# Kernel tuning notes

Measured on AMD Instinct MI355X. Metric: run time of the kernel, lower is better.

The kernel has to match this reference:

```python
import jax, jax.numpy as jnp
import numpy as np

HIDDEN_DIM = 1024
SEQ_LEN = 4096
D_IN = 1024


def setup_inputs() -> dict:
    key = jax.random.key(0)
    ks = jax.random.split(key, 9)
    s = 1.0 / np.sqrt(D_IN)
    return {
        "q": jax.random.normal(ks[0], (SEQ_LEN, D_IN), jnp.float32),
        "k": jax.random.normal(ks[1], (SEQ_LEN, D_IN), jnp.float32),
        "v": jax.random.normal(ks[2], (SEQ_LEN, D_IN), jnp.float32),
        "Wq": jax.random.normal(ks[3], (D_IN, HIDDEN_DIM), jnp.float32) * s,
        "bq": jnp.zeros((HIDDEN_DIM,), jnp.float32),
        "Wk": jax.random.normal(ks[4], (D_IN, HIDDEN_DIM), jnp.float32) * s,
        "bk": jnp.zeros((HIDDEN_DIM,), jnp.float32),
        "Wv": jax.random.normal(ks[5], (D_IN, HIDDEN_DIM), jnp.float32) * s,
        "bv": jnpp_zeros() if False else jnp.zeros((HIDDEN_DIM,), jnp.float32),
    }


def reference(q, k, v, Wq, bq, Wk, bk, Wv, bv):
    # Dense projections (flax Dense: x @ W + b)
    query = q @ Wq + bq          # [S, H]
    key_p = k @ Wk + bk          # [S, H]
    value = v @ Wv + bv          # [S, H]
    # scores = Q K^T / sqrt(hidden_dim)  -> [S, S]
    scores = jnp.matmul(query, key_p.T) / jnp.sqrt(jnp.float32(HIDDEN_DIM))
    weights = jax.nn.softmax(scores, axis=-1)
    context = jnp.matmul(weights, value)  # [S, H]
    return context
```

## Files before the change

### kernel.cpp

```cpp
#include <hip/hip_runtime.h>


typedef short short4v __attribute__((ext_vector_type(4)));
typedef short short8  __attribute__((ext_vector_type(8)));
typedef float f32x4   __attribute__((ext_vector_type(4)));

#define MFMA16 __builtin_amdgcn_mfma_f32_16x16x32_bf16

__device__ __forceinline__ short f2bf(float f) {
    union { float f; unsigned u; } x; x.f = f;
    unsigned r = (x.u + 0x7FFFu + ((x.u >> 16) & 1u)) >> 16;
    return (short)r;
}
__device__ __forceinline__ float bf2f(short s) {
    union { unsigned u; float f; } x;
    x.u = ((unsigned)(unsigned short)s) << 16; return x.f;
}
__device__ __forceinline__ void store_out(short* p, float v) { *p = f2bf(v); }
__device__ __forceinline__ void store_out(float* p, float v) { *p = v; }

__device__ __forceinline__ void gl2lds(const short* g, short* l) {
    __builtin_amdgcn_global_load_lds(
        (const __attribute__((address_space(1))) void*)g,
        (__attribute__((address_space(3))) void*)l, 16, 0, 0);
}

__global__ __launch_bounds__(256) void prep_w(
    const float* __restrict__ W0, const float* __restrict__ W1,
    const float* __restrict__ W2, short* __restrict__ Wt)
{
    __shared__ float tile[64][65];
    const float* W = blockIdx.z == 0 ? W0 : (blockIdx.z == 1 ? W1 : W2);
    short* T = Wt + (size_t)blockIdx.z * 1048576;
    const int c0 = blockIdx.x * 64;
    const int r0 = blockIdx.y * 64;
    const int tx = threadIdx.x & 63;
    const int ty = threadIdx.x >> 6;
    #pragma unroll
    for (int p = 0; p < 16; ++p) {
        int r = ty + p * 4;
        tile[r][tx] = W[(size_t)(r0 + r) * 1024 + c0 + tx];
    }
    __syncthreads();
    #pragma unroll
    for (int p = 0; p < 16; ++p) {
        int r = ty + p * 4;
        T[(size_t)(c0 + r) * 1024 + r0 + tx] = f2bf(tile[tx][r]);
    }
}

__global__ __launch_bounds__(256) void cast_qkv(
    const float* __restrict__ q, const float* __restrict__ k,
    const float* __restrict__ v, short* __restrict__ xb)
{
    const float* src = blockIdx.z == 0 ? q : (blockIdx.z == 1 ? k : v);
    short* dst = xb + (size_t)blockIdx.z * 4194304;
    for (int i = blockIdx.x * 256 + threadIdx.x; i < 1048576; i += 256 * 1024) {
        float4 f = ((const float4*)src)[i];
        short4v o;
        o[0] = f2bf(f.x); o[1] = f2bf(f.y); o[2] = f2bf(f.z); o[3] = f2bf(f.w);
        ((short4v*)dst)[i] = o;
    }
}

__global__ __launch_bounds__(256) void transpose_v(
    const short* __restrict__ src, short* __restrict__ dst)
{
    __shared__ short t[64][65];
    const int c0 = blockIdx.x * 64;
    const int r0 = blockIdx.y * 64;
    const int tx = threadIdx.x & 63;
    const int ty = threadIdx.x >> 6;
    #pragma unroll
    for (int p = 0; p < 16; ++p) {
        const int r = p * 4 + ty;
        t[r][tx] = src[(size_t)(r0 + r) * 1024 + c0 + tx];
    }
    __syncthreads();
    #pragma unroll
    for (int p = 0; p < 16; ++p) {
        const int r = p * 4 + ty;
        dst[(size_t)(c0 + r) * 4096 + r0 + tx] = t[tx][r];
    }
}

template <typename TOut, int MODE>
__global__ __launch_bounds__(512, 2) void gemm256(
    const short* __restrict__ A, const short* __restrict__ Bt,
    const float* __restrict__ b0, const float* __restrict__ b1,
    const float* __restrict__ b2,
    TOut* __restrict__ C, float* __restrict__ P1, float* __restrict__ P2,
    float* __restrict__ P3,
    int M, int N, int lda, int ldb, float scale,
    int nc, int nc_last, int kstep)
{
    __shared__ short Lds[65536];

    const int t    = threadIdx.x;
    const int lane = t & 63;
    const int wv   = t >> 6;

    int m0, n0;
    {
        const int nb  = gridDim.x;
        const int bid = blockIdx.y * nb + blockIdx.x;
        if (nb == 16 && gridDim.y == 16) {
            const int x = bid & 7, i = bid >> 3;
            m0 = ((x & 1) * 8 + (i & 7)) * 256;
            n0 = ((x >> 1) * 4 + (i >> 3)) * 256;
        } else {
            const int band   = bid / (8 * nb);
            const int within = bid - band * 8 * nb;
            m0 = (band * 8 + (within & 7)) * 256;
            n0 = (within >> 3) * 256;
        }
    }

    const float* bias = nullptr;
    int kbeg = 0;
    TOut* Cw = C;
    if constexpr (MODE == 1) {
        const int z = blockIdx.z;
        A  += (size_t)z * M * lda;
        Bt += (size_t)z * N * ldb;
        Cw  = C + (size_t)z * M * N;
        bias = z == 0 ? b0 : (z == 1 ? b1 : b2);
    }
    if constexpr (MODE == 2) {
        const int z = blockIdx.z;
        kbeg = z * kstep;
        if (z == (int)gridDim.z - 1) nc = nc_last;
        Cw = (TOut*)(z == 0 ? (float*)C : (z == 1 ? P1 : (z == 2 ? P2 : P3)));
    }
    (void)b0; (void)b1; (void)b2; (void)P1; (void)P2; (void)P3;
    (void)nc_last; (void)kstep;

    const int srow = lane >> 2;
    const int skof = (lane & 3) * 8;
    const short* pA0 = A  + (size_t)(m0 + wv * 16 + srow) * lda + kbeg + skof;
    const short* pA1 = pA0 + (size_t)128 * lda;
    const short* pB0 = Bt + (size_t)(n0 + wv * 16 + srow) * ldb + kbeg + skof;
    const short* pB1 = pB0 + (size_t)128 * ldb;
    short* sA0 = Lds + wv * 512;
    short* sA1 = Lds + 4096  + wv * 512;
    short* sB0 = Lds + 8192  + wv * 512;
    short* sB1 = Lds + 12288 + wv * 512;

    const int wm = wv >> 2, wn = wv & 3;
    const int lr = lane & 15, lq = lane >> 4;
    const short* rdA = Lds + (wm * 128 + lr) * 32 + lq * 8;
    const short* rdB = Lds + 8192 + (wn * 64 + lr) * 32 + lq * 8;

    f32x4 acc[8][4];
    #pragma unroll
    for (int i = 0; i < 8; ++i)
        #pragma unroll
        for (int j = 0; j < 4; ++j) { f32x4 z4 = {0.f,0.f,0.f,0.f}; acc[i][j] = z4; }

#define STAGE(c) {                                                        \
    const int su_ = (c) & 3;                                              \
    const size_t ko_ = (size_t)(c) * 32;                                  \
    gl2lds(pA0 + ko_, sA0 + su_ * 16384);                                 \
    gl2lds(pA1 + ko_, sA1 + su_ * 16384);                                 \
    gl2lds(pB0 + ko_, sB0 + su_ * 16384);                                 \
    gl2lds(pB1 + ko_, sB1 + su_ * 16384); }

    STAGE(0); STAGE(1); STAGE(2);
    asm volatile("s_waitcnt vmcnt(8)" ::: "memory");
    __builtin_amdgcn_s_barrier();

#define PHASE(c, DOSTAGE, VMN) {                                          \
    const int u_ = (c) & 3;                                               \
    const short* rA_ = rdA + u_ * 16384;                                  \
    const short* rB_ = rdB + u_ * 16384;                                  \
    short8 af[8], bfr[4];                                                 \
    _Pragma("unroll") for (int i = 0; i < 8; ++i)                         \
        af[i] = *(const short8*)(rA_ + i * 512);                          \
    _Pragma("unroll") for (int j = 0; j < 4; ++j)                         \
        bfr[j] = *(const short8*)(rB_ + j * 512);                         \
    if (DOSTAGE) STAGE((c) + 3);                                          \
    __builtin_amdgcn_s_barrier();                                         \
    __builtin_amdgcn_s_setprio(1);                                        \
    _Pragma("unroll") for (int i = 0; i < 8; ++i)                         \
        _Pragma("unroll") for (int j = 0; j < 4; ++j)                     \
            acc[i][j] = MFMA16(af[i], bfr[j], acc[i][j], 0, 0, 0);        \
    __builtin_amdgcn_s_setprio(0);                                        \
    if ((VMN) == 8)      asm volatile("s_waitcnt vmcnt(8)" ::: "memory"); \
    else if ((VMN) == 4) asm volatile("s_waitcnt vmcnt(4)" ::: "memory"); \
    else if ((VMN) == 0) asm volatile("s_waitcnt vmcnt(0)" ::: "memory"); \
    if ((VMN) >= 0) __builtin_amdgcn_s_barrier(); }

    #pragma unroll 4
    for (int c = 0; c < nc - 3; ++c) PHASE(c, 1, 8);
    PHASE(nc - 3, 0, 4);
    PHASE(nc - 2, 0, 0);
    PHASE(nc - 1, 0, -1);
#undef PHASE
#undef STAGE

    #pragma unroll
    for (int i = 0; i < 8; ++i) {
        const int crow = m0 + wm * 128 + i * 16 + lq * 4;
        #pragma unroll
        for (int j = 0; j < 4; ++j) {
            const int ccol = n0 + wn * 64 + j * 16 + lr;
            float bb = 0.f;
            if constexpr (MODE == 1) bb = bias[ccol];
            #pragma unroll
            for (int r = 0; r < 4; ++r) {
                float val = acc[i][j][r] * scale + bb;
                store_out(&Cw[(size_t)(crow + r) * N + ccol], val);
            }
        }
    }
}

__global__ __launch_bounds__(256) void softmax_bf16(short* __restrict__ S)
{
    const int row = blockIdx.x;
    short8* r8 = (short8*)(S + (size_t)row * 4096);
    const int t = threadIdx.x;

    float x[16];
    #pragma unroll
    for (int i = 0; i < 2; ++i) {
        short8 raw = r8[t + 256 * i];
        #pragma unroll
        for (int j = 0; j < 8; ++j) x[8 * i + j] = bf2f(raw[j]);
    }
    float m = -1e30f;
    #pragma unroll
    for (int i = 0; i < 16; ++i) m = fmaxf(m, x[i]);
    #pragma unroll
    for (int off = 32; off > 0; off >>= 1) m = fmaxf(m, __shfl_xor(m, off));

    __shared__ float redm[4], reds[4];
    const int wv = t >> 6;
    if ((t & 63) == 0) redm[wv] = m;
    __syncthreads();
    m = fmaxf(fmaxf(redm[0], redm[1]), fmaxf(redm[2], redm[3]));

    float s = 0.f;
    #pragma unroll
    for (int i = 0; i < 16; ++i) { x[i] = __expf(x[i] - m); s += x[i]; }
    #pragma unroll
    for (int off = 32; off > 0; off >>= 1) s += __shfl_xor(s, off);
    if ((t & 63) == 0) reds[wv] = s;
    __syncthreads();
    s = reds[0] + reds[1] + reds[2] + reds[3];
    const float inv = 1.f / s;

    #pragma unroll
    for (int i = 0; i < 2; ++i) {
        short8 o;
        #pragma unroll
        for (int j = 0; j < 8; ++j) o[j] = f2bf(x[8 * i + j] * inv);
        r8[t + 256 * i] = o;
    }
}

__global__ __launch_bounds__(256) void combine(
    float* __restrict__ out, const float* __restrict__ a,
    const float* __restrict__ b, const float* __restrict__ c, int np)
{
    for (int i = blockIdx.x * 256 + threadIdx.x; i < 1048576; i += 256 * 1024) {
        float4 o = ((const float4*)out)[i];
        float4 x = ((const float4*)a)[i];
        float4 y = ((const float4*)b)[i];
        o.x += x.x + y.x; o.y += x.y + y.y;
        o.z += x.z + y.z; o.w += x.w + y.w;
        if (np == 3) {
            float4 w = ((const float4*)c)[i];
            o.x += w.x; o.y += w.y; o.z += w.z; o.w += w.w;
        }
        ((float4*)out)[i] = o;
    }
}

extern "C" void kernel_launch(void* const* d_in, const int* in_sizes, int n_in,
                              void* d_out, int out_size, void* d_ws, size_t ws_size,
                              hipStream_t stream)
{
    const float* q  = (const float*)d_in[0];
    const float* k  = (const float*)d_in[1];
    const float* v  = (const float*)d_in[2];
    const float* Wq = (const float*)d_in[3];
    const float* bq = (const float*)d_in[4];
    const float* Wk = (const float*)d_in[5];
    const float* bk = (const float*)d_in[6];
    const float* Wv = (const float*)d_in[7];
    const float* bv = (const float*)d_in[8];
    float* out = (float*)d_out;

    char* ws = (char*)d_ws;
    const size_t MB = 1ull << 20;
    short* Wt = (short*)(ws + 0);
    short* xb = (short*)(ws + 6 * MB);
    short* pr = (short*)(ws + 30 * MB);
    short* S  = (short*)(ws + 46 * MB);
    short* Vt = (short*)(ws + 78 * MB);
    float* p1 = (float*)(ws + 0);
    float* p2 = (float*)(ws + 16 * MB);
    float* p3 = (float*)(ws + 86 * MB);
    const int SK = (ws_size >= 102 * MB) ? 4 : 3;

    prep_w<<<dim3(16, 16, 3), 256, 0, stream>>>(Wq, Wk, Wv, Wt);
    cast_qkv<<<dim3(1024, 1, 3), 256, 0, stream>>>(q, k, v, xb);
    gemm256<short, 1><<<dim3(4, 16, 3), 512, 0, stream>>>(
        xb, Wt, bq, bk, bv, pr, nullptr, nullptr, nullptr,
        4096, 1024, 1024, 1024, 1.f, 32, 32, 0);
    transpose_v<<<dim3(16, 64), 256, 0, stream>>>(pr + 8 * 1024 * 1024, Vt);
    gemm256<short, 0><<<dim3(16, 16), 512, 0, stream>>>(
        pr, pr + 4 * 1024 * 1024, nullptr, nullptr, nullptr, S,
        nullptr, nullptr, nullptr,
        4096, 4096, 1024, 1024, 0.03125f, 32, 32, 0);
    softmax_bf16<<<4096, 256, 0, stream>>>(S);
    if (SK == 4) {
        gemm256<float, 2><<<dim3(4, 16, 4), 512, 0, stream>>>(
            S, Vt, nullptr, nullptr, nullptr, out, p1, p2, p3,
            4096, 1024, 4096, 4096, 1.f, 32, 32, 1024);
        combine<<<1024, 256, 0, stream>>>(out, p1, p2, p3, 3);
    } else {
        gemm256<float, 2><<<dim3(4, 16, 3), 512, 0, stream>>>(
            S, Vt, nullptr, nullptr, nullptr, out, p1, p2, nullptr,
            4096, 1024, 4096, 4096, 1.f, 42, 44, 1344);
        combine<<<1024, 256, 0, stream>>>(out, p1, p2, nullptr, 2);
    }
}
```

Baseline: 259.6 us.

## Swizzle LDS tile layout and split GEMM phase into two half-A MFMA sub-phases

Applies an XOR swizzle to the 16-byte chunk column used by both the global-to-LDS loads and the LDS fragment reads, so fragment reads from LDS avoid bank conflicts. Each pipeline phase is also split into two halves. The first half loads four A fragments and issues the A prefetch, and the second half reloads the other four A fragments and issues the B prefetch. This cuts live fragment registers and interleaves global loads with MFMA work, at the cost of extra barriers per phase.

```diff
diff --git a/kernel.cpp b/kernel.cpp
--- a/kernel.cpp
+++ b/kernel.cpp
@@ -136,7 +136,7 @@
     (void)nc_last; (void)kstep;
 
     const int srow = lane >> 2;
-    const int skof = (lane & 3) * 8;
+    const int skof = ((lane & 3) ^ ((lane >> 3) & 3)) * 8;
     const short* pA0 = A  + (size_t)(m0 + wv * 16 + srow) * lda + kbeg + skof;
     const short* pA1 = pA0 + (size_t)128 * lda;
     const short* pB0 = Bt + (size_t)(n0 + wv * 16 + srow) * ldb + kbeg + skof;
@@ -148,8 +148,9 @@
 
     const int wm = wv >> 2, wn = wv & 3;
     const int lr = lane & 15, lq = lane >> 4;
-    const short* rdA = Lds + (wm * 128 + lr) * 32 + lq * 8;
-    const short* rdB = Lds + 8192 + (wn * 64 + lr) * 32 + lq * 8;
+    const int pcol = lq ^ ((lr >> 1) & 3);
+    const short* rdA = Lds + (wm * 128 + lr) * 32 + pcol * 8;
+    const short* rdB = Lds + 8192 + (wn * 64 + lr) * 32 + pcol * 8;
 
     f32x4 acc[8][4];
     #pragma unroll
@@ -157,15 +158,20 @@
         #pragma unroll
         for (int j = 0; j < 4; ++j) { f32x4 z4 = {0.f,0.f,0.f,0.f}; acc[i][j] = z4; }
 
-#define STAGE(c) {                                                        \
+#define STAGE_A(c) {                                                      \
     const int su_ = (c) & 3;                                              \
     const size_t ko_ = (size_t)(c) * 32;                                  \
     gl2lds(pA0 + ko_, sA0 + su_ * 16384);                                 \
-    gl2lds(pA1 + ko_, sA1 + su_ * 16384);                                 \
+    gl2lds(pA1 + ko_, sA1 + su_ * 16384); }
+#define STAGE_B(c) {                                                      \
+    const int su_ = (c) & 3;                                              \
+    const size_t ko_ = (size_t)(c) * 32;                                  \
     gl2lds(pB0 + ko_, sB0 + su_ * 16384);                                 \
     gl2lds(pB1 + ko_, sB1 + su_ * 16384); }
 
-    STAGE(0); STAGE(1); STAGE(2);
+    STAGE_A(0); STAGE_B(0);
+    STAGE_A(1); STAGE_B(1);
+    STAGE_A(2); STAGE_B(2);
     asm volatile("s_waitcnt vmcnt(8)" ::: "memory");
     __builtin_amdgcn_s_barrier();
 
@@ -173,17 +179,27 @@
     const int u_ = (c) & 3;                                               \
     const short* rA_ = rdA + u_ * 16384;                                  \
     const short* rB_ = rdB + u_ * 16384;                                  \
-    short8 af[8], bfr[4];                                                 \
-    _Pragma("unroll") for (int i = 0; i < 8; ++i)                         \
+    short8 af[4], bfr[4];                                                 \
+    _Pragma("unroll") for (int i = 0; i < 4; ++i)                         \
         af[i] = *(const short8*)(rA_ + i * 512);                          \
     _Pragma("unroll") for (int j = 0; j < 4; ++j)                         \
         bfr[j] = *(const short8*)(rB_ + j * 512);                         \
-    if (DOSTAGE) STAGE((c) + 3);                                          \
+    if (DOSTAGE) STAGE_A((c) + 3);                                        \
     __builtin_amdgcn_s_barrier();                                         \
     __builtin_amdgcn_s_setprio(1);                                        \
-    _Pragma("unroll") for (int i = 0; i < 8; ++i)                         \
+    _Pragma("unroll") for (int i = 0; i < 4; ++i)                         \
         _Pragma("unroll") for (int j = 0; j < 4; ++j)                     \
             acc[i][j] = MFMA16(af[i], bfr[j], acc[i][j], 0, 0, 0);        \
+    __builtin_amdgcn_s_setprio(0);                                        \
+    __builtin_amdgcn_s_barrier();                                         \
+    _Pragma("unroll") for (int i = 0; i < 4; ++i)                         \
+        af[i] = *(const short8*)(rA_ + (4 + i) * 512);                    \
+    if (DOSTAGE) STAGE_B((c) + 3);                                        \
+    __builtin_amdgcn_s_barrier();                                         \
+    __builtin_amdgcn_s_setprio(1);                                        \
+    _Pragma("unroll") for (int i = 0; i < 4; ++i)                         \
+        _Pragma("unroll") for (int j = 0; j < 4; ++j)                     \
+            acc[4 + i][j] = MFMA16(af[i], bfr[j], acc[4 + i][j], 0, 0, 0);\
     __builtin_amdgcn_s_setprio(0);                                        \
     if ((VMN) == 8)      asm volatile("s_waitcnt vmcnt(8)" ::: "memory"); \
     else if ((VMN) == 4) asm volatile("s_waitcnt vmcnt(4)" ::: "memory"); \
@@ -196,7 +212,8 @@
     PHASE(nc - 2, 0, 0);
     PHASE(nc - 1, 0, -1);
 #undef PHASE
-#undef STAGE
+#undef STAGE_A
+#undef STAGE_B
 
     #pragma unroll
     for (int i = 0; i < 8; ++i) {
```

Measured after the change: 253.3 us. -2.4%, faster.

## Shrink GEMM tile to 128x256 with double buffering and swizzled LDS

Applied to the files above, without the earlier changes.

Replaces the 256x256 GEMM tile with a 128x256 tile and cuts the accumulator array in half. The four-stage LDS ring becomes a two-stage double buffer using much less shared memory, and launch bounds rise to allow four blocks per CU. LDS column offsets are XOR-swizzled on both the write and read side to reduce bank conflicts. Grids double in the M dimension to give more blocks and better occupancy, at the cost of less data reuse per block, a shallower prefetch pipeline, and dropping the special 16x16 block-order remap used for the scores GEMM.

```diff
diff --git a/kernel.cpp b/kernel.cpp
--- a/kernel.cpp
+++ b/kernel.cpp
@@ -85,7 +85,7 @@
 }
 
 template <typename TOut, int MODE>
-__global__ __launch_bounds__(512, 2) void gemm256(
+__global__ __launch_bounds__(512, 4) void gemm128(
     const short* __restrict__ A, const short* __restrict__ Bt,
     const float* __restrict__ b0, const float* __restrict__ b1,
     const float* __restrict__ b2,
@@ -94,27 +94,18 @@
     int M, int N, int lda, int ldb, float scale,
     int nc, int nc_last, int kstep)
 {
-    __shared__ short Lds[65536];
+    __shared__ short Lds[24576];
 
     const int t    = threadIdx.x;
     const int lane = t & 63;
     const int wv   = t >> 6;
 
-    int m0, n0;
-    {
-        const int nb  = gridDim.x;
-        const int bid = blockIdx.y * nb + blockIdx.x;
-        if (nb == 16 && gridDim.y == 16) {
-            const int x = bid & 7, i = bid >> 3;
-            m0 = ((x & 1) * 8 + (i & 7)) * 256;
-            n0 = ((x >> 1) * 4 + (i >> 3)) * 256;
-        } else {
-            const int band   = bid / (8 * nb);
-            const int within = bid - band * 8 * nb;
-            m0 = (band * 8 + (within & 7)) * 256;
-            n0 = (within >> 3) * 256;
-        }
-    }
+    const int nb  = gridDim.x;
+    const int bid = blockIdx.y * nb + blockIdx.x;
+    const int band   = bid / (8 * nb);
+    const int within = bid - band * 8 * nb;
+    const int m0 = (band * 8 + (within & 7)) * 128;
+    const int n0 = (within >> 3) * 256;
 
     const float* bias = nullptr;
     int kbeg = 0;
@@ -136,71 +127,65 @@
     (void)nc_last; (void)kstep;
 
     const int srow = lane >> 2;
-    const int skof = (lane & 3) * 8;
-    const short* pA0 = A  + (size_t)(m0 + wv * 16 + srow) * lda + kbeg + skof;
-    const short* pA1 = pA0 + (size_t)128 * lda;
+    const int skof = ((lane & 3) ^ ((lane >> 3) & 3)) * 8;
+    const short* pA  = A  + (size_t)(m0 + wv * 16 + srow) * lda + kbeg + skof;
     const short* pB0 = Bt + (size_t)(n0 + wv * 16 + srow) * ldb + kbeg + skof;
     const short* pB1 = pB0 + (size_t)128 * ldb;
-    short* sA0 = Lds + wv * 512;
-    short* sA1 = Lds + 4096  + wv * 512;
-    short* sB0 = Lds + 8192  + wv * 512;
-    short* sB1 = Lds + 12288 + wv * 512;
+    short* sA  = Lds + wv * 512;
+    short* sB0 = Lds + 4096 + wv * 512;
+    short* sB1 = Lds + 8192 + wv * 512;
 
     const int wm = wv >> 2, wn = wv & 3;
     const int lr = lane & 15, lq = lane >> 4;
-    const short* rdA = Lds + (wm * 128 + lr) * 32 + lq * 8;
-    const short* rdB = Lds + 8192 + (wn * 64 + lr) * 32 + lq * 8;
-
-    f32x4 acc[8][4];
-    #pragma unroll
-    for (int i = 0; i < 8; ++i)
+    const int pcol = lq ^ ((lr >> 1) & 3);
+    const short* rdA = Lds + (wm * 64 + lr) * 32 + pcol * 8;
+    const short* rdB = Lds + 4096 + (wn * 64 + lr) * 32 + pcol * 8;
+
+    f32x4 acc[4][4];
+    #pragma unroll
+    for (int i = 0; i < 4; ++i)
         #pragma unroll
         for (int j = 0; j < 4; ++j) { f32x4 z4 = {0.f,0.f,0.f,0.f}; acc[i][j] = z4; }
 
 #define STAGE(c) {                                                        \
-    const int su_ = (c) & 3;                                              \
+    const int s_ = (c) & 1;                                               \
     const size_t ko_ = (size_t)(c) * 32;                                  \
-    gl2lds(pA0 + ko_, sA0 + su_ * 16384);                                 \
-    gl2lds(pA1 + ko_, sA1 + su_ * 16384);                                 \
-    gl2lds(pB0 + ko_, sB0 + su_ * 16384);                                 \
-    gl2lds(pB1 + ko_, sB1 + su_ * 16384); }
-
-    STAGE(0); STAGE(1); STAGE(2);
-    asm volatile("s_waitcnt vmcnt(8)" ::: "memory");
-    __builtin_amdgcn_s_barrier();
-
-#define PHASE(c, DOSTAGE, VMN) {                                          \
-    const int u_ = (c) & 3;                                               \
-    const short* rA_ = rdA + u_ * 16384;                                  \
-    const short* rB_ = rdB + u_ * 16384;                                  \
-    short8 af[8], bfr[4];                                                 \
-    _Pragma("unroll") for (int i = 0; i < 8; ++i)                         \
+    gl2lds(pA  + ko_, sA  + s_ * 12288);                                  \
+    gl2lds(pB0 + ko_, sB0 + s_ * 12288);                                  \
+    gl2lds(pB1 + ko_, sB1 + s_ * 12288); }
+
+#define COMPUTE(c) {                                                      \
+    const short* rA_ = rdA + ((c) & 1) * 12288;                           \
+    const short* rB_ = rdB + ((c) & 1) * 12288;                           \
+    short8 af[4], bf_[4];                                                 \
+    _Pragma("unroll") for (int i = 0; i < 4; ++i)                         \
         af[i] = *(const short8*)(rA_ + i * 512);                          \
     _Pragma("unroll") for (int j = 0; j < 4; ++j)                         \
-        bfr[j] = *(const short8*)(rB_ + j * 512);                         \
-    if (DOSTAGE) STAGE((c) + 3);                                          \
-    __builtin_amdgcn_s_barrier();                                         \
+        bf_[j] = *(const short8*)(rB_ + j * 512);                         \
     __builtin_amdgcn_s_setprio(1);                                        \
-    _Pragma("unroll") for (int i = 0; i < 8; ++i)                         \
+    _Pragma("unroll") for (int i = 0; i < 4; ++i)                         \
         _Pragma("unroll") for (int j = 0; j < 4; ++j)                     \
-            acc[i][j] = MFMA16(af[i], bfr[j], acc[i][j], 0, 0, 0);        \
-    __builtin_amdgcn_s_setprio(0);                                        \
-    if ((VMN) == 8)      asm volatile("s_waitcnt vmcnt(8)" ::: "memory"); \
-    else if ((VMN) == 4) asm volatile("s_waitcnt vmcnt(4)" ::: "memory"); \
-    else if ((VMN) == 0) asm volatile("s_waitcnt vmcnt(0)" ::: "memory"); \
-    if ((VMN) >= 0) __builtin_amdgcn_s_barrier(); }
-
-    #pragma unroll 4
-    for (int c = 0; c < nc - 3; ++c) PHASE(c, 1, 8);
-    PHASE(nc - 3, 0, 4);
-    PHASE(nc - 2, 0, 0);
-    PHASE(nc - 1, 0, -1);
-#undef PHASE
+            acc[i][j] = MFMA16(af[i], bf_[j], acc[i][j], 0, 0, 0);        \
+    __builtin_amdgcn_s_setprio(0); }
+
+    STAGE(0);
+
+    for (int c = 0; c < nc - 1; ++c) {
+        STAGE(c + 1);
+        asm volatile("s_waitcnt vmcnt(3)" ::: "memory");
+        __builtin_amdgcn_s_barrier();
+        COMPUTE(c);
+        __builtin_amdgcn_s_barrier();
+    }
+    asm volatile("s_waitcnt vmcnt(0)" ::: "memory");
+    __builtin_amdgcn_s_barrier();
+    COMPUTE(nc - 1);
+#undef COMPUTE
 #undef STAGE
 
     #pragma unroll
-    for (int i = 0; i < 8; ++i) {
-        const int crow = m0 + wm * 128 + i * 16 + lq * 4;
+    for (int i = 0; i < 4; ++i) {
+        const int crow = m0 + wm * 64 + i * 16 + lq * 4;
         #pragma unroll
         for (int j = 0; j < 4; ++j) {
             const int ccol = n0 + wn * 64 + j * 16 + lr;
@@ -306,22 +291,22 @@
 
     prep_w<<<dim3(16, 16, 3), 256, 0, stream>>>(Wq, Wk, Wv, Wt);
     cast_qkv<<<dim3(1024, 1, 3), 256, 0, stream>>>(q, k, v, xb);
-    gemm256<short, 1><<<dim3(4, 16, 3), 512, 0, stream>>>(
+    gemm128<short, 1><<<dim3(4, 32, 3), 512, 0, stream>>>(
         xb, Wt, bq, bk, bv, pr, nullptr, nullptr, nullptr,
         4096, 1024, 1024, 1024, 1.f, 32, 32, 0);
     transpose_v<<<dim3(16, 64), 256, 0, stream>>>(pr + 8 * 1024 * 1024, Vt);
-    gemm256<short, 0><<<dim3(16, 16), 512, 0, stream>>>(
+    gemm128<short, 0><<<dim3(16, 32), 512, 0, stream>>>(
         pr, pr + 4 * 1024 * 1024, nullptr, nullptr, nullptr, S,
         nullptr, nullptr, nullptr,
         4096, 4096, 1024, 1024, 0.03125f, 32, 32, 0);
     softmax_bf16<<<4096, 256, 0, stream>>>(S);
     if (SK == 4) {
-        gemm256<float, 2><<<dim3(4, 16, 4), 512, 0, stream>>>(
+        gemm128<float, 2><<<dim3(4, 32, 4), 512, 0, stream>>>(
             S, Vt, nullptr, nullptr, nullptr, out, p1, p2, p3,
             4096, 1024, 4096, 4096, 1.f, 32, 32, 1024);
         combine<<<1024, 256, 0, stream>>>(out, p1, p2, p3, 3);
     } else {
-        gemm256<float, 2><<<dim3(4, 16, 3), 512, 0, stream>>>(
+        gemm128<float, 2><<<dim3(4, 32, 3), 512, 0, stream>>>(
             S, Vt, nullptr, nullptr, nullptr, out, p1, p2, nullptr,
             4096, 1024, 4096, 4096, 1.f, 42, 44, 1344);
         combine<<<1024, 256, 0, stream>>>(out, p1, p2, nullptr, 2);
```

Result: faster. 254.2 us (-2.1%).
